# Optimization experiments

Hardware: AMD Instinct MI355X
Metric: run time of the kernel (lower is better)

Reference implementation:

```python
import jax, jax.numpy as jnp
import numpy as np

HEADS = 8
DIM_HEAD = 64
SCALE = DIM_HEAD ** (-0.5)


def setup_inputs() -> dict:
    key = jax.random.key(0)
    k1, k2, k3 = jax.random.split(key, 3)
    b, l, c = 8, 4096, 512
    x = jax.random.normal(k1, (b, l, c), dtype=jnp.float32)
    w_qkv = jax.random.normal(k2, (3 * c, c), dtype=jnp.float32) * (c ** -0.5)
    w_out = jax.random.normal(k3, (c, c), dtype=jnp.float32) * (c ** -0.5)
    b_out = jnp.zeros((c,), dtype=jnp.float32)
    return {"x": x, "w_qkv": w_qkv, "w_out": w_out, "b_out": b_out}


def reference(x, w_qkv, w_out, b_out):
    b, l, c = x.shape
    h = HEADS
    lh = l // h
    # to_qkv: Linear(dim, 3*dim, bias=False)
    qkv = x @ w_qkv.T                                   # (b, l, 3c)
    qkv = qkv.reshape(b, lh, h, 3, c).transpose(3, 0, 2, 1, 4)  # (3, b, h, l/h, c)
    q, k, v = qkv[0], qkv[1], qkv[2]                    # each (b, h, l/h, c)
    # transpose(-2,-1): attention is over the CHANNEL axis
    q = jnp.swapaxes(q, -2, -1)                         # (b, h, c, l/h)
    k = jnp.swapaxes(k, -2, -1)                         # (b, h, c, l/h)
    v = jnp.swapaxes(v, -2, -1)                         # (b, h, c, l/h)
    attn = jnp.einsum('bhcl,bhdl->bhcd', q, k) * SCALE  # (b, h, c, c)
    attn = jax.nn.softmax(attn, axis=-1)
    y = jnp.einsum('bhcd,bhdl->bhcl', attn, v)          # (b, h, c, l/h)
    y = y.transpose(0, 3, 1, 2).reshape(b, l, c)        # (b, l/h, h, c) -> (b, l, c)
    # to_out: Linear(dim, dim) + Dropout (identity at eval)
    out = y @ w_out.T + b_out
    return out
```

## Files before the change

### kernel.cpp

```cpp
#include <hip/hip_runtime.h>
#include <stdint.h>
#include <stddef.h>

typedef _Float16 f16;
typedef _Float16 f16x8 __attribute__((ext_vector_type(8)));
typedef _Float16 f16x4 __attribute__((ext_vector_type(4)));
typedef float f32x4 __attribute__((ext_vector_type(4)));

__device__ __forceinline__ void gload16(const void* g, void* l) {
    auto gp = (const __attribute__((address_space(1))) uint32_t*)(uintptr_t)g;
    auto lp = (__attribute__((address_space(3))) uint32_t*)(uintptr_t)l;
    __builtin_amdgcn_global_load_lds(gp, lp, 16, 0, 0);
}

__device__ __forceinline__ f16x4 cvt4(f32x4 v) {
    return f16x4{ (f16)v[0], (f16)v[1], (f16)v[2], (f16)v[3] };
}

__global__ __launch_bounds__(256) void prep_k(const float* __restrict__ x,
                                              const float* __restrict__ wqkv,
                                              const float* __restrict__ wout,
                                              f16* __restrict__ xb,
                                              f16* __restrict__ wqb,
                                              f16* __restrict__ wob) {
    int tid = blockIdx.x * blockDim.x + threadIdx.x;
    int stride = gridDim.x * blockDim.x;
    for (int i = tid; i < 4194304; i += stride) {
        float4 v = ((const float4*)x)[i];
        *(f16x4*)(xb + (size_t)i * 4) = f16x4{ (f16)v.x, (f16)v.y, (f16)v.z, (f16)v.w };
    }
    for (int i = tid; i < 196608; i += stride) {
        float4 v = ((const float4*)wqkv)[i];
        *(f16x4*)(wqb + (size_t)i * 4) = f16x4{ (f16)v.x, (f16)v.y, (f16)v.z, (f16)v.w };
    }
    for (int i = tid; i < 65536; i += stride) {
        float4 v = ((const float4*)wout)[i];
        *(f16x4*)(wob + (size_t)i * 4) = f16x4{ (f16)v.x, (f16)v.y, (f16)v.z, (f16)v.w };
    }
}

#define W0  asm volatile("s_waitcnt vmcnt(0)" ::: "memory")
#define BAR __builtin_amdgcn_s_barrier()


#define A_STAGE(NB) do {                                                        \
    gload16(Ab + kb + sE,          &ldsA[NB][( 0 + wid*8)*64]);                 \
    gload16(Ab + kb + sO + 32768,  &ldsA[NB][(32 + wid*8)*64]);                 \
    gload16(Ab + kb + sE + 65536,  &ldsA[NB][(64 + wid*8)*64]);                 \
    gload16(Ab + kb + sO + 98304,  &ldsA[NB][(96 + wid*8)*64]);                 \
    gload16(Bb + kb + sE,          &ldsB[NB][( 0 + wid*8)*64]);                 \
    gload16(Bb + kb + sO + 32768,  &ldsB[NB][(32 + wid*8)*64]);                 \
    gload16(Bb + kb + sE + 65536,  &ldsB[NB][(64 + wid*8)*64]);                 \
    gload16(Bb + kb + sO + 98304,  &ldsB[NB][(96 + wid*8)*64]);                 \
    kb += 128;                                                                  \
} while (0)

#define A_RD(SET, BUF) do {                                                     \
    _Pragma("unroll") for (int mi = 0; mi < 4; ++mi)                            \
    _Pragma("unroll") for (int kk = 0; kk < 2; ++kk)                            \
        aF##SET[mi][kk] = *(const f16x8*)(&ldsA[BUF][0] + aoff[mi][kk]);        \
    _Pragma("unroll") for (int ni = 0; ni < 4; ++ni)                            \
    _Pragma("unroll") for (int kk = 0; kk < 2; ++kk)                            \
        bF##SET[ni][kk] = *(const f16x8*)(&ldsB[BUF][0] + boff[ni][kk]);        \
} while (0)

#define A_MM(SET, KK, ML, MH_) do {                                             \
    __builtin_amdgcn_s_setprio(1);                                              \
    _Pragma("unroll") for (int mi = ML; mi < MH_; ++mi)                         \
    _Pragma("unroll") for (int ni = 0; ni < 4; ++ni) {                          \
        if constexpr (SWP)                                                      \
            acc[mi][ni] = __builtin_amdgcn_mfma_f32_16x16x32_f16(               \
                bF##SET[ni][KK], aF##SET[mi][KK], acc[mi][ni], 0, 0, 0);        \
        else                                                                    \
            acc[mi][ni] = __builtin_amdgcn_mfma_f32_16x16x32_f16(               \
                aF##SET[mi][KK], bF##SET[ni][KK], acc[mi][ni], 0, 0, 0);        \
    }                                                                           \
    __builtin_amdgcn_s_setprio(0);                                              \
} while (0)

#define A_MM3(SET)   do { A_MM(SET, 0, 0, 2); A_MM(SET, 0, 2, 4); A_MM(SET, 1, 0, 2); } while (0)
#define A_MMLAST(SET) A_MM(SET, 1, 2, 4)

#define A_TILE(CUR, NXT, NB, STG, FINAL) do {                                   \
    if (STG) A_STAGE(NB);                                                       \
    A_MM3(CUR);                                                                 \
    if (!FINAL) { W0; BAR; A_RD(NXT, NB); }                                     \
    A_MMLAST(CUR);                                                              \
} while (0)

template <int MODE, bool SWP, bool QK>
__global__ __launch_bounds__(256, 2) void g10_k(const f16* __restrict__ A0,
                                                const f16* __restrict__ B0,
                                                void* __restrict__ C0,
                                                void* __restrict__ C1,
                                                const float* __restrict__ bias) {
    __shared__ f16 ldsA[2][8192];
    __shared__ f16 ldsB[2][8192];

    const int tid = threadIdx.x;
    const int lane = tid & 63;
    const int wid = tid >> 6;
    const int wr = wid >> 1;
    const int wc = wid & 1;

    const int bid = blockIdx.x;
    int tm, tn;
    if constexpr (MODE == 0 && QK) {
        int swz = (bid & 7) * 256 + (bid >> 3);
        tm = (swz >> 3) * 128; tn = (swz & 7) * 128;
    } else {
        int swz = (bid & 7) * 128 + (bid >> 3);
        tm = (swz >> 2) * 128; tn = (swz & 3) * 128;
    }

    const char* Ab = (const char*)(A0 + (size_t)tm * 512);
    const char* Bb = (const char*)(B0 + (size_t)tn * 512);

    const int u = tid >> 3;
    const int colE = ((tid & 7) ^ ((u & 7) ^ (u >> 3))) * 16;
    const int sE = u * 1024 + colE;
    const int sO = sE ^ 64;
    int kb = 0;

    int aoff[4][2], boff[4][2];
#pragma unroll
    for (int mi = 0; mi < 4; ++mi) {
        int r;
        if constexpr (QK) {
            r = (lane & 15) * 8 + wr * 4 + mi;
        } else {
            r = wr * 64 + mi * 16 + (lane & 15);
        }
#pragma unroll
        for (int kk = 0; kk < 2; ++kk) {
            int c8 = (lane >> 4) + kk * 4;
            aoff[mi][kk] = r * 64 + (c8 ^ ((r & 7) ^ ((r >> 3) & 7))) * 8;
        }
    }
#pragma unroll
    for (int ni = 0; ni < 4; ++ni) {
        int r = wc * 64 + ni * 16 + (lane & 15);
#pragma unroll
        for (int kk = 0; kk < 2; ++kk) {
            int c8 = (lane >> 4) + kk * 4;
            boff[ni][kk] = r * 64 + (c8 ^ ((r & 7) ^ ((r >> 3) & 7))) * 8;
        }
    }

    f32x4 acc[4][4] = {};
    f16x8 aF0[4][2], bF0[4][2], aF1[4][2], bF1[4][2];

    A_STAGE(0);
    W0; BAR;
    A_RD(0, 0);

#pragma unroll 1
    for (int i = 0; i < 3; ++i) {
        A_TILE(0, 1, 1, true, false);
        A_TILE(1, 0, 0, true, false);
    }
    A_TILE(0, 1, 1, true, false);
    A_TILE(1, 1, 1, false, true);

    if constexpr (MODE == 0 && QK) {
        const int b = tm >> 12;
        const int lt = (tm & 4095) >> 3;
        f16* dst = (f16*)(tn < 512 ? C0 : C1);
        const int cb = (tn & 511) + wc * 64;
        const int lh0 = lt + (lane >> 4) * 4;
#pragma unroll
        for (int mi = 0; mi < 4; ++mi) {
            int h = wr * 4 + mi;
#pragma unroll
            for (int ni = 0; ni < 4; ++ni) {
                int c = cb + ni * 16 + (lane & 15);
                *(f16x4*)(dst + ((size_t)((b * 8 + h) * 512 + c)) * 512 + lh0) =
                    cvt4(acc[mi][ni]);
            }
        }
    } else {
        f16* dst = (f16*)C0;
#pragma unroll
        for (int mi = 0; mi < 4; ++mi) {
            int t = tm + wr * 64 + mi * 16 + (lane & 15);
            int b = t >> 12, l = t & 4095;
            int h = l & 7, lh = l >> 3;
#pragma unroll
            for (int ni = 0; ni < 4; ++ni) {
                int d0 = tn + wc * 64 + ni * 16 + (lane >> 4) * 4;
                *(f16x4*)(dst + ((size_t)((b * 8 + h) * 512 + lh)) * 512 + d0) =
                    cvt4(acc[mi][ni]);
            }
        }
    }
}


#define S_STAGE(B) do {                                                         \
    gload16(Qt + kb + soff,           &ldsQ[B][(  0 + wid*8)*64]);              \
    gload16(Qt + kb + soff + 65536,   &ldsQ[B][( 64 + wid*8)*64]);              \
    gload16(Kt + kb + soff,           &ldsK[B][(  0 + wid*8)*64]);              \
    gload16(Kt + kb + soff + 65536,   &ldsK[B][( 64 + wid*8)*64]);              \
    gload16(Kt + kb + soff + 131072,  &ldsK[B][(128 + wid*8)*64]);              \
    gload16(Kt + kb + soff + 196608,  &ldsK[B][(192 + wid*8)*64]);              \
    gload16(Kt + kb + soff + 262144,  &ldsK[B][(256 + wid*8)*64]);              \
    gload16(Kt + kb + soff + 327680,  &ldsK[B][(320 + wid*8)*64]);              \
    gload16(Kt + kb + soff + 393216,  &ldsK[B][(384 + wid*8)*64]);              \
    gload16(Kt + kb + soff + 458752,  &ldsK[B][(448 + wid*8)*64]);              \
    kb += 128;                                                                  \
} while (0)

#define S_RD(KK, B) do {                                                        \
    _Pragma("unroll") for (int ni = 0; ni < 4; ++ni)                            \
        bF[ni] = *(const f16x8*)(&ldsK[B][0] + boff[ni][KK]);                   \
    _Pragma("unroll") for (int mi = 0; mi < 8; ++mi)                            \
        aF[mi] = *(const f16x8*)(&ldsQ[B][0] + aoff[mi][KK]);                   \
} while (0)

#define S_MM do {                                                               \
    __builtin_amdgcn_s_setprio(1);                                              \
    _Pragma("unroll") for (int mi = 0; mi < 8; ++mi)                            \
    _Pragma("unroll") for (int ni = 0; ni < 4; ++ni)                            \
        acc[mi][ni] = __builtin_amdgcn_mfma_f32_16x16x32_f16(                   \
            aF[mi], bF[ni], acc[mi][ni], 0, 0, 0);                              \
    __builtin_amdgcn_s_setprio(0);                                              \
} while (0)

__global__ __launch_bounds__(512) void sfm_k(const f16* __restrict__ Qb,
                                             const f16* __restrict__ Kb,
                                             f16* __restrict__ Pb) {
    __shared__ f16 ldsQ[2][8192];
    __shared__ f16 ldsK[2][32768];

    const int tid = threadIdx.x;
    const int lane = tid & 63;
    const int wid = tid >> 6;
    const int g = lane >> 4;
    const int li = lane & 15;

    const int bid = blockIdx.x;
    const int swz = (bid & 7) * 32 + (bid >> 3);
    const int bh = swz >> 2, ct = swz & 3;

    const char* Qt = (const char*)(Qb + (size_t)bh * 262144 + (size_t)ct * 128 * 512);
    const char* Kt = (const char*)(Kb + (size_t)bh * 262144);

    const int soff = (tid >> 3) * 1024 +
                     ((((lane & 7) ^ (lane >> 3) ^ wid) & 7) * 16);
    int kb = 0;

    int aoff[8][2], boff[4][2];
#pragma unroll
    for (int mi = 0; mi < 8; ++mi) {
        int r = mi * 16 + li;
        int s3 = (r & 7) ^ ((r >> 3) & 7);
#pragma unroll
        for (int kk = 0; kk < 2; ++kk)
            aoff[mi][kk] = r * 64 + (((g + kk * 4) ^ s3)) * 8;
    }
#pragma unroll
    for (int ni = 0; ni < 4; ++ni) {
        int r = wid * 64 + ni * 16 + li;
        int s3 = (r & 7) ^ ((r >> 3) & 7);
#pragma unroll
        for (int kk = 0; kk < 2; ++kk)
            boff[ni][kk] = r * 64 + (((g + kk * 4) ^ s3)) * 8;
    }

    f32x4 acc[8][4] = {};
    f16x8 aF[8], bF[4];

    S_STAGE(0);
#pragma unroll 1
    for (int t = 0; t < 8; ++t) {
        const int cb = t & 1;
        if (t < 7) {
            S_STAGE(cb ^ 1);
            asm volatile("s_waitcnt vmcnt(10)" ::: "memory");
        } else {
            W0;
        }
        BAR;
        S_RD(0, cb);
        S_MM;
        S_RD(1, cb);
        S_MM;
        BAR;
    }

    float* red  = (float*)&ldsQ[0][0];
    float* redg = (float*)&ldsK[0][0];

#pragma unroll
    for (int mi = 0; mi < 8; ++mi)
#pragma unroll
        for (int ni = 0; ni < 4; ++ni) acc[mi][ni] *= 0.125f;

#pragma unroll
    for (int mi = 0; mi < 8; ++mi)
#pragma unroll
        for (int j = 0; j < 4; ++j) {
            float v = fmaxf(fmaxf(acc[mi][0][j], acc[mi][1][j]),
                            fmaxf(acc[mi][2][j], acc[mi][3][j]));
#pragma unroll
            for (int off = 1; off < 16; off <<= 1) v = fmaxf(v, __shfl_xor(v, off, 64));
            if (li == 0) red[wid * 128 + mi * 16 + g * 4 + j] = v;
        }
    BAR;
    if (tid < 128) {
        float m = red[tid];
#pragma unroll
        for (int w = 1; w < 8; ++w) m = fmaxf(m, red[w * 128 + tid]);
        redg[tid] = m;
    }
    BAR;

#pragma unroll
    for (int mi = 0; mi < 8; ++mi)
#pragma unroll
        for (int j = 0; j < 4; ++j) {
            float mg = redg[mi * 16 + g * 4 + j];
            float s = 0.f;
#pragma unroll
            for (int ni = 0; ni < 4; ++ni) {
                float e = __expf(acc[mi][ni][j] - mg);
                acc[mi][ni][j] = e;
                s += e;
            }
#pragma unroll
            for (int off = 1; off < 16; off <<= 1) s += __shfl_xor(s, off, 64);
            if (li == 0) red[wid * 128 + mi * 16 + g * 4 + j] = s;
        }
    BAR;
    if (tid < 128) {
        float s = red[tid];
#pragma unroll
        for (int w = 1; w < 8; ++w) s += red[w * 128 + tid];
        redg[tid] = 1.0f / s;
    }
    BAR;

    f16* Pt = Pb + (size_t)bh * 262144;
#pragma unroll
    for (int mi = 0; mi < 8; ++mi)
#pragma unroll
        for (int j = 0; j < 4; ++j) {
            int row = mi * 16 + g * 4 + j;
            float is = redg[row];
            size_t base = (size_t)(ct * 128 + row) * 512 + wid * 64 + li;
#pragma unroll
            for (int ni = 0; ni < 4; ++ni)
                Pt[base + ni * 16] = (f16)(acc[mi][ni][j] * is);
        }
}


#define B_STAGE(NB) do {                                                        \
    gload16(At + soff,          &ldsA2[NB][(  0 + wid*8)*64]);                  \
    gload16(At + soff + 65536,  &ldsA2[NB][( 64 + wid*8)*64]);                  \
    gload16(At + soff + 131072, &ldsA2[NB][(128 + wid*8)*64]);                  \
    gload16(At + soff + 196608, &ldsA2[NB][(192 + wid*8)*64]);                  \
    gload16(Bt + soff,          &ldsB2[NB][(  0 + wid*8)*64]);                  \
    gload16(Bt + soff + 65536,  &ldsB2[NB][( 64 + wid*8)*64]);                  \
    gload16(Bt + soff + 131072, &ldsB2[NB][(128 + wid*8)*64]);                  \
    gload16(Bt + soff + 196608, &ldsB2[NB][(192 + wid*8)*64]);                  \
    At += 128; Bt += 128;                                                       \
} while (0)

#define B_RD12(KK, BUF) do {                                                    \
    _Pragma("unroll") for (int ni = 0; ni < 4; ++ni)                            \
        bF[ni] = *(const f16x8*)(&ldsB2[BUF][0] + boff[ni][KK]);                \
    _Pragma("unroll") for (int mi = 0; mi < 8; ++mi)                            \
        aF[mi] = *(const f16x8*)(&ldsA2[BUF][0] + aoff[mi][KK]);                \
} while (0)

#define B_MM32 do {                                                             \
    __builtin_amdgcn_s_setprio(1);                                              \
    _Pragma("unroll") for (int mi = 0; mi < 8; ++mi)                            \
    _Pragma("unroll") for (int ni = 0; ni < 4; ++ni) {                          \
        if constexpr (SWP)                                                      \
            acc[mi][ni] = __builtin_amdgcn_mfma_f32_16x16x32_f16(               \
                bF[ni], aF[mi], acc[mi][ni], 0, 0, 0);                          \
        else                                                                    \
            acc[mi][ni] = __builtin_amdgcn_mfma_f32_16x16x32_f16(               \
                aF[mi], bF[ni], acc[mi][ni], 0, 0, 0);                          \
    }                                                                           \
    __builtin_amdgcn_s_setprio(0);                                              \
} while (0)

#define B_TILE(CB, NB, STG, FINAL) do {                                         \
    B_RD12(0, CB);                                                              \
    if (STG) B_STAGE(NB);                                                       \
    B_MM32;                                                                     \
    B_RD12(1, CB);                                                              \
    B_MM32;                                                                     \
    if (!FINAL) { W0; BAR; }                                                    \
} while (0)

template <int MODE, bool SWP>
__global__ __launch_bounds__(512) void g12_k(const f16* __restrict__ A0,
                                             const f16* __restrict__ B0,
                                             void* __restrict__ C0,
                                             const float* __restrict__ bias) {
    __shared__ f16 ldsA2[2][16384];
    __shared__ f16 ldsB2[2][16384];

    const int tid = threadIdx.x;
    const int lane = tid & 63;
    const int wid = tid >> 6;
    const int wr = wid >> 2;
    const int wc = wid & 3;

    const int bid = blockIdx.x;
    int tm, tn, bh = 0;
    if constexpr (MODE == 2) {
        int swz = (bid & 7) * 32 + (bid >> 3);
        bh = swz >> 2; tm = ((swz >> 1) & 1) * 256; tn = (swz & 1) * 256;
    } else {
        int swz = (bid & 7) * 32 + (bid >> 3);
        tm = (swz >> 1) * 256; tn = (swz & 1) * 256;
    }

    const size_t bhoff = (MODE == 2) ? (size_t)bh * 262144 : 0;
    const char* At = (const char*)(A0 + bhoff + (size_t)tm * 512);
    const char* Bt = (const char*)(B0 + bhoff + (size_t)tn * 512);

    const int soff = wid * 8192 + (lane >> 3) * 1024 +
                     ((((lane & 7) ^ (lane >> 3) ^ wid) & 7) * 16);

    int aoff[8][2], boff[4][2];
#pragma unroll
    for (int mi = 0; mi < 8; ++mi) {
        int r = wr * 128 + mi * 16 + (lane & 15);
        int s3 = (r & 7) ^ ((r >> 3) & 7);
#pragma unroll
        for (int kk = 0; kk < 2; ++kk)
            aoff[mi][kk] = r * 64 + ((((lane >> 4) + kk * 4) ^ s3)) * 8;
    }
#pragma unroll
    for (int ni = 0; ni < 4; ++ni) {
        int r = wc * 64 + ni * 16 + (lane & 15);
        int s3 = (r & 7) ^ ((r >> 3) & 7);
#pragma unroll
        for (int kk = 0; kk < 2; ++kk)
            boff[ni][kk] = r * 64 + ((((lane >> 4) + kk * 4) ^ s3)) * 8;
    }

    f32x4 acc[8][4] = {};
    f16x8 aF[8], bF[4];

    B_STAGE(0);
    W0; BAR;

#pragma unroll 1
    for (int i = 0; i < 3; ++i) {
        B_TILE(0, 1, true, false);
        B_TILE(1, 0, true, false);
    }
    B_TILE(0, 1, true, false);
    B_TILE(1, 1, false, true);

    if constexpr (MODE == 2) {
        f16* yb = (f16*)C0;
        const int b = bh >> 3, h = bh & 7;
#pragma unroll
        for (int mi = 0; mi < 8; ++mi) {
            int c0 = tm + wr * 128 + mi * 16 + (lane >> 4) * 4;
#pragma unroll
            for (int ni = 0; ni < 4; ++ni) {
                int l = tn + wc * 64 + ni * 16 + (lane & 15);
                size_t tok = (size_t)b * 4096 + (size_t)l * 8 + h;
                *(f16x4*)(yb + tok * 512 + c0) = cvt4(acc[mi][ni]);
            }
        }
    } else {
        float* O = (float*)C0;
#pragma unroll
        for (int mi = 0; mi < 8; ++mi) {
            int m = tm + wr * 128 + mi * 16 + (lane & 15);
#pragma unroll
            for (int ni = 0; ni < 4; ++ni) {
                int n0 = tn + wc * 64 + ni * 16 + (lane >> 4) * 4;
                float4 bv = *(const float4*)(bias + n0);
                f32x4 v = acc[mi][ni];
                v[0] += bv.x; v[1] += bv.y; v[2] += bv.z; v[3] += bv.w;
                *(f32x4*)(O + (size_t)m * 512 + n0) = v;
            }
        }
    }
}

extern "C" void kernel_launch(void* const* d_in, const int* in_sizes, int n_in,
                              void* d_out, int out_size, void* d_ws, size_t ws_size,
                              hipStream_t stream) {
    const float* x = (const float*)d_in[0];
    const float* wqkv = (const float*)d_in[1];
    const float* wout = (const float*)d_in[2];
    const float* bout = (const float*)d_in[3];
    float* out = (float*)d_out;
    char* ws = (char*)d_ws;
    const size_t MBs = 1u << 20;

    f16* xb  = (f16*)(ws + 0);
    f16* wqb = (f16*)(ws + 32 * MBs);
    f16* wob = (f16*)(ws + 34 * MBs);
    f16* Qb  = (f16*)(ws + 35 * MBs);
    f16* Kb  = (f16*)(ws + 67 * MBs);
    f16* Vb  = (f16*)(ws + 99 * MBs);
    f16* Pb  = xb;
    f16* yb  = Qb;

    prep_k<<<1024, 256, 0, stream>>>(x, wqkv, wout, xb, wqb, wob);
    g10_k<0, false, true><<<2048, 256, 0, stream>>>(xb, wqb, Qb, Kb, nullptr);
    g10_k<0, true, false><<<1024, 256, 0, stream>>>(xb, wqb + (size_t)1024 * 512, Vb, nullptr, nullptr);
    sfm_k<<<256, 512, 0, stream>>>(Qb, Kb, Pb);
    g12_k<2, false><<<256, 512, 0, stream>>>(Pb, Vb, yb, nullptr);
    g12_k<3, true><<<256, 512, 0, stream>>>(yb, wob, out, bout);
}
```

Measured before the change: 190.5 us.

## Load weight operand directly from global into registers, drop B LDS staging

The 128x128 GEMM kernel no longer stages the weight (B) operand through shared memory. Each lane now loads its B fragments straight from global memory into a double-buffered register set, one tile ahead, which halves LDS footprint and LDS read traffic. The output projection also moves from the 256x256-tile kernel to this 128x128 kernel with 1024 blocks. The cost is more VGPRs and uncoalesced, L2-dependent global reads for B, and the global-load latency is only hidden by one tile of prefetch.

Result: slower. 254.0 us (+33.3%).

```diff
diff --git a/kernel.cpp b/kernel.cpp
--- a/kernel.cpp
+++ b/kernel.cpp
@@ -43,65 +43,66 @@
 #define BAR __builtin_amdgcn_s_barrier()
 
 
-#define A_STAGE(NB) do {                                                        \
+#define D_STAGE(NB) do {                                                        \
     gload16(Ab + kb + sE,          &ldsA[NB][( 0 + wid*8)*64]);                 \
     gload16(Ab + kb + sO + 32768,  &ldsA[NB][(32 + wid*8)*64]);                 \
     gload16(Ab + kb + sE + 65536,  &ldsA[NB][(64 + wid*8)*64]);                 \
     gload16(Ab + kb + sO + 98304,  &ldsA[NB][(96 + wid*8)*64]);                 \
-    gload16(Bb + kb + sE,          &ldsB[NB][( 0 + wid*8)*64]);                 \
-    gload16(Bb + kb + sO + 32768,  &ldsB[NB][(32 + wid*8)*64]);                 \
-    gload16(Bb + kb + sE + 65536,  &ldsB[NB][(64 + wid*8)*64]);                 \
-    gload16(Bb + kb + sO + 98304,  &ldsB[NB][(96 + wid*8)*64]);                 \
     kb += 128;                                                                  \
 } while (0)
 
-#define A_RD(SET, BUF) do {                                                     \
+#define D_LOADB(SET) do {                                                       \
+    _Pragma("unroll") for (int ni = 0; ni < 4; ++ni)                            \
+    _Pragma("unroll") for (int kk = 0; kk < 2; ++kk)                            \
+        bG##SET[ni][kk] = *(const f16x8*)(Bg + vb[ni] + kk * 64);               \
+    Bg += 128;                                                                  \
+} while (0)
+
+#define D_RDA(SET, BUF) do {                                                    \
     _Pragma("unroll") for (int mi = 0; mi < 4; ++mi)                            \
     _Pragma("unroll") for (int kk = 0; kk < 2; ++kk)                            \
         aF##SET[mi][kk] = *(const f16x8*)(&ldsA[BUF][0] + aoff[mi][kk]);        \
-    _Pragma("unroll") for (int ni = 0; ni < 4; ++ni)                            \
-    _Pragma("unroll") for (int kk = 0; kk < 2; ++kk)                            \
-        bF##SET[ni][kk] = *(const f16x8*)(&ldsB[BUF][0] + boff[ni][kk]);        \
-} while (0)
-
-#define A_MM(SET, KK, ML, MH_) do {                                             \
+} while (0)
+
+#define D_MM(SET, KK, ML, MH_) do {                                             \
     __builtin_amdgcn_s_setprio(1);                                              \
     _Pragma("unroll") for (int mi = ML; mi < MH_; ++mi)                         \
     _Pragma("unroll") for (int ni = 0; ni < 4; ++ni) {                          \
         if constexpr (SWP)                                                      \
             acc[mi][ni] = __builtin_amdgcn_mfma_f32_16x16x32_f16(               \
-                bF##SET[ni][KK], aF##SET[mi][KK], acc[mi][ni], 0, 0, 0);        \
+                bG##SET[ni][KK], aF##SET[mi][KK], acc[mi][ni], 0, 0, 0);        \
         else                                                                    \
             acc[mi][ni] = __builtin_amdgcn_mfma_f32_16x16x32_f16(               \
-                aF##SET[mi][KK], bF##SET[ni][KK], acc[mi][ni], 0, 0, 0);        \
+                aF##SET[mi][KK], bG##SET[ni][KK], acc[mi][ni], 0, 0, 0);        \
     }                                                                           \
     __builtin_amdgcn_s_setprio(0);                                              \
 } while (0)
 
-#define A_MM3(SET)   do { A_MM(SET, 0, 0, 2); A_MM(SET, 0, 2, 4); A_MM(SET, 1, 0, 2); } while (0)
-#define A_MMLAST(SET) A_MM(SET, 1, 2, 4)
-
-#define A_TILE(CUR, NXT, NB, STG, FINAL) do {                                   \
-    if (STG) A_STAGE(NB);                                                       \
-    A_MM3(CUR);                                                                 \
-    if (!FINAL) { W0; BAR; A_RD(NXT, NB); }                                     \
-    A_MMLAST(CUR);                                                              \
+#define D_MM3(SET)   do { D_MM(SET, 0, 0, 2); D_MM(SET, 0, 2, 4); D_MM(SET, 1, 0, 2); } while (0)
+#define D_MMLAST(SET) D_MM(SET, 1, 2, 4)
+
+#define D_TILE(CUR, NXT, NB, STG, FINAL) do {                                   \
+    if (STG) { D_STAGE(NB); D_LOADB(NXT); }                                     \
+    D_MM3(CUR);                                                                 \
+    if (!FINAL) { W0; BAR; D_RDA(NXT, NB); }                                    \
+    D_MMLAST(CUR);                                                              \
 } while (0)
 
 template <int MODE, bool SWP, bool QK>
-__global__ __launch_bounds__(256, 2) void g10_k(const f16* __restrict__ A0,
+__global__ __launch_bounds__(256, 2) void g14_k(const f16* __restrict__ A0,
                                                 const f16* __restrict__ B0,
                                                 void* __restrict__ C0,
                                                 void* __restrict__ C1,
                                                 const float* __restrict__ bias) {
     __shared__ f16 ldsA[2][8192];
-    __shared__ f16 ldsB[2][8192];
 
     const int tid = threadIdx.x;
     const int lane = tid & 63;
     const int wid = tid >> 6;
     const int wr = wid >> 1;
     const int wc = wid & 1;
+    const int g = lane >> 4;
+    const int li = lane & 15;
 
     const int bid = blockIdx.x;
     int tm, tn;
@@ -114,7 +115,7 @@
     }
 
     const char* Ab = (const char*)(A0 + (size_t)tm * 512);
-    const char* Bb = (const char*)(B0 + (size_t)tn * 512);
+    const char* Bg = (const char*)(B0 + (size_t)tn * 512);
 
     const int u = tid >> 3;
     const int colE = ((tid & 7) ^ ((u & 7) ^ (u >> 3))) * 16;
@@ -122,79 +123,89 @@
     const int sO = sE ^ 64;
     int kb = 0;
 
-    int aoff[4][2], boff[4][2];
+    int vb[4];
+#pragma unroll
+    for (int ni = 0; ni < 4; ++ni)
+        vb[ni] = (wc * 64 + ni * 16 + li) * 1024 + g * 16;
+
+    int aoff[4][2];
 #pragma unroll
     for (int mi = 0; mi < 4; ++mi) {
         int r;
         if constexpr (QK) {
-            r = (lane & 15) * 8 + wr * 4 + mi;
+            r = li * 8 + wr * 4 + mi;
         } else {
-            r = wr * 64 + mi * 16 + (lane & 15);
+            r = wr * 64 + mi * 16 + li;
         }
 #pragma unroll
         for (int kk = 0; kk < 2; ++kk) {
-            int c8 = (lane >> 4) + kk * 4;
+            int c8 = g + kk * 4;
             aoff[mi][kk] = r * 64 + (c8 ^ ((r & 7) ^ ((r >> 3) & 7))) * 8;
         }
     }
-#pragma unroll
-    for (int ni = 0; ni < 4; ++ni) {
-        int r = wc * 64 + ni * 16 + (lane & 15);
-#pragma unroll
-        for (int kk = 0; kk < 2; ++kk) {
-            int c8 = (lane >> 4) + kk * 4;
-            boff[ni][kk] = r * 64 + (c8 ^ ((r & 7) ^ ((r >> 3) & 7))) * 8;
-        }
-    }
 
     f32x4 acc[4][4] = {};
-    f16x8 aF0[4][2], bF0[4][2], aF1[4][2], bF1[4][2];
-
-    A_STAGE(0);
+    f16x8 aF0[4][2], aF1[4][2], bG0[4][2], bG1[4][2];
+
+    D_STAGE(0);
+    D_LOADB(0);
     W0; BAR;
-    A_RD(0, 0);
+    D_RDA(0, 0);
 
 #pragma unroll 1
     for (int i = 0; i < 3; ++i) {
-        A_TILE(0, 1, 1, true, false);
-        A_TILE(1, 0, 0, true, false);
-    }
-    A_TILE(0, 1, 1, true, false);
-    A_TILE(1, 1, 1, false, true);
+        D_TILE(0, 1, 1, true, false);
+        D_TILE(1, 0, 0, true, false);
+    }
+    D_TILE(0, 1, 1, true, false);
+    D_TILE(1, 1, 1, false, true);
 
     if constexpr (MODE == 0 && QK) {
         const int b = tm >> 12;
         const int lt = (tm & 4095) >> 3;
         f16* dst = (f16*)(tn < 512 ? C0 : C1);
         const int cb = (tn & 511) + wc * 64;
-        const int lh0 = lt + (lane >> 4) * 4;
+        const int lh0 = lt + g * 4;
 #pragma unroll
         for (int mi = 0; mi < 4; ++mi) {
             int h = wr * 4 + mi;
 #pragma unroll
             for (int ni = 0; ni < 4; ++ni) {
-                int c = cb + ni * 16 + (lane & 15);
+                int c = cb + ni * 16 + li;
                 *(f16x4*)(dst + ((size_t)((b * 8 + h) * 512 + c)) * 512 + lh0) =
                     cvt4(acc[mi][ni]);
             }
         }
-    } else {
+    } else if constexpr (MODE == 0) {
         f16* dst = (f16*)C0;
 #pragma unroll
         for (int mi = 0; mi < 4; ++mi) {
-            int t = tm + wr * 64 + mi * 16 + (lane & 15);
+            int t = tm + wr * 64 + mi * 16 + li;
             int b = t >> 12, l = t & 4095;
             int h = l & 7, lh = l >> 3;
 #pragma unroll
             for (int ni = 0; ni < 4; ++ni) {
-                int d0 = tn + wc * 64 + ni * 16 + (lane >> 4) * 4;
+                int d0 = tn + wc * 64 + ni * 16 + g * 4;
                 *(f16x4*)(dst + ((size_t)((b * 8 + h) * 512 + lh)) * 512 + d0) =
                     cvt4(acc[mi][ni]);
             }
         }
-    }
-}
-
+    } else {
+        float* O = (float*)C0;
+#pragma unroll
+        for (int mi = 0; mi < 4; ++mi) {
+            int m = tm + wr * 64 + mi * 16 + li;
+#pragma unroll
+            for (int ni = 0; ni < 4; ++ni) {
+                int n0 = tn + wc * 64 + ni * 16 + g * 4;
+                float4 bv = *(const float4*)(bias + n0);
+                f32x4 v = acc[mi][ni];
+                v[0] += bv.x; v[1] += bv.y; v[2] += bv.z; v[3] += bv.w;
+                *(f32x4*)(O + (size_t)m * 512 + n0) = v;
+            }
+        }
+    }
+}
 
 #define S_STAGE(B) do {                                                         \
     gload16(Qt + kb + soff,           &ldsQ[B][(  0 + wid*8)*64]);              \
@@ -354,7 +365,6 @@
         }
 }
 
-
 #define B_STAGE(NB) do {                                                        \
     gload16(At + soff,          &ldsA2[NB][(  0 + wid*8)*64]);                  \
     gload16(At + soff + 65536,  &ldsA2[NB][( 64 + wid*8)*64]);                  \
@@ -377,14 +387,9 @@
 #define B_MM32 do {                                                             \
     __builtin_amdgcn_s_setprio(1);                                              \
     _Pragma("unroll") for (int mi = 0; mi < 8; ++mi)                            \
-    _Pragma("unroll") for (int ni = 0; ni < 4; ++ni) {                          \
-        if constexpr (SWP)                                                      \
-            acc[mi][ni] = __builtin_amdgcn_mfma_f32_16x16x32_f16(               \
-                bF[ni], aF[mi], acc[mi][ni], 0, 0, 0);                          \
-        else                                                                    \
-            acc[mi][ni] = __builtin_amdgcn_mfma_f32_16x16x32_f16(               \
-                aF[mi], bF[ni], acc[mi][ni], 0, 0, 0);                          \
-    }                                                                           \
+    _Pragma("unroll") for (int ni = 0; ni < 4; ++ni)                            \
+        acc[mi][ni] = __builtin_amdgcn_mfma_f32_16x16x32_f16(                   \
+            aF[mi], bF[ni], acc[mi][ni], 0, 0, 0);                              \
     __builtin_amdgcn_s_setprio(0);                                              \
 } while (0)
 
@@ -397,11 +402,9 @@
     if (!FINAL) { W0; BAR; }                                                    \
 } while (0)
 
-template <int MODE, bool SWP>
-__global__ __launch_bounds__(512) void g12_k(const f16* __restrict__ A0,
-                                             const f16* __restrict__ B0,
-                                             void* __restrict__ C0,
-                                             const float* __restrict__ bias) {
+__global__ __launch_bounds__(512) void pv_k(const f16* __restrict__ A0,
+                                            const f16* __restrict__ B0,
+                                            f16* __restrict__ C0) {
     __shared__ f16 ldsA2[2][16384];
     __shared__ f16 ldsB2[2][16384];
 
@@ -412,16 +415,10 @@
     const int wc = wid & 3;
 
     const int bid = blockIdx.x;
-    int tm, tn, bh = 0;
-    if constexpr (MODE == 2) {
-        int swz = (bid & 7) * 32 + (bid >> 3);
-        bh = swz >> 2; tm = ((swz >> 1) & 1) * 256; tn = (swz & 1) * 256;
-    } else {
-        int swz = (bid & 7) * 32 + (bid >> 3);
-        tm = (swz >> 1) * 256; tn = (swz & 1) * 256;
-    }
-
-    const size_t bhoff = (MODE == 2) ? (size_t)bh * 262144 : 0;
+    int swz = (bid & 7) * 32 + (bid >> 3);
+    int bh = swz >> 2, tm = ((swz >> 1) & 1) * 256, tn = (swz & 1) * 256;
+
+    const size_t bhoff = (size_t)bh * 262144;
     const char* At = (const char*)(A0 + bhoff + (size_t)tm * 512);
     const char* Bt = (const char*)(B0 + bhoff + (size_t)tn * 512);
 
@@ -460,32 +457,16 @@
     B_TILE(0, 1, true, false);
     B_TILE(1, 1, false, true);
 
-    if constexpr (MODE == 2) {
-        f16* yb = (f16*)C0;
-        const int b = bh >> 3, h = bh & 7;
-#pragma unroll
-        for (int mi = 0; mi < 8; ++mi) {
-            int c0 = tm + wr * 128 + mi * 16 + (lane >> 4) * 4;
-#pragma unroll
-            for (int ni = 0; ni < 4; ++ni) {
-                int l = tn + wc * 64 + ni * 16 + (lane & 15);
-                size_t tok = (size_t)b * 4096 + (size_t)l * 8 + h;
-                *(f16x4*)(yb + tok * 512 + c0) = cvt4(acc[mi][ni]);
-            }
-        }
-    } else {
-        float* O = (float*)C0;
-#pragma unroll
-        for (int mi = 0; mi < 8; ++mi) {
-            int m = tm + wr * 128 + mi * 16 + (lane & 15);
-#pragma unroll
-            for (int ni = 0; ni < 4; ++ni) {
-                int n0 = tn + wc * 64 + ni * 16 + (lane >> 4) * 4;
-                float4 bv = *(const float4*)(bias + n0);
-                f32x4 v = acc[mi][ni];
-                v[0] += bv.x; v[1] += bv.y; v[2] += bv.z; v[3] += bv.w;
-                *(f32x4*)(O + (size_t)m * 512 + n0) = v;
-            }
+    f16* yb = C0;
+    const int b = bh >> 3, h = bh & 7;
+#pragma unroll
+    for (int mi = 0; mi < 8; ++mi) {
+        int c0 = tm + wr * 128 + mi * 16 + (lane >> 4) * 4;
+#pragma unroll
+        for (int ni = 0; ni < 4; ++ni) {
+            int l = tn + wc * 64 + ni * 16 + (lane & 15);
+            size_t tok = (size_t)b * 4096 + (size_t)l * 8 + h;
+            *(f16x4*)(yb + tok * 512 + c0) = cvt4(acc[mi][ni]);
         }
     }
 }
@@ -511,9 +492,9 @@
     f16* yb  = Qb;
 
     prep_k<<<1024, 256, 0, stream>>>(x, wqkv, wout, xb, wqb, wob);
-    g10_k<0, false, true><<<2048, 256, 0, stream>>>(xb, wqb, Qb, Kb, nullptr);
-    g10_k<0, true, false><<<1024, 256, 0, stream>>>(xb, wqb + (size_t)1024 * 512, Vb, nullptr, nullptr);
+    g14_k<0, false, true><<<2048, 256, 0, stream>>>(xb, wqb, Qb, Kb, nullptr);
+    g14_k<0, true, false><<<1024, 256, 0, stream>>>(xb, wqb + (size_t)1024 * 512, Vb, nullptr, nullptr);
     sfm_k<<<256, 512, 0, stream>>>(Qb, Kb, Pb);
-    g12_k<2, false><<<256, 512, 0, stream>>>(Pb, Vb, yb, nullptr);
-    g12_k<3, true><<<256, 512, 0, stream>>>(yb, wob, out, bout);
-}
+    pv_k<<<256, 512, 0, stream>>>(Pb, Vb, yb);
+    g14_k<3, true, false><<<1024, 256, 0, stream>>>(yb, wob, out, nullptr, bout);
+}
```
